# Performance work log

Hardware: AMD Instinct MI355X
Metric: run time of the kernel (lower is better)

Reference implementation:

```python
import jax, jax.numpy as jnp
import numpy as np

FIELD = 32
DIM = 64
LAYER_SIZE = (128, 128)


def setup_inputs() -> dict:
    key = jax.random.key(0)
    ks = jax.random.split(key, 5)
    B = 4096
    x = jax.random.normal(ks[0], (B, FIELD, DIM), dtype=jnp.float32)
    # conv1d kernel-size-1 weights, stored as [out_channels, in_channels]
    field_nums = [FIELD]
    params = {}
    for i, size in enumerate(LAYER_SIZE):
        in_ch = field_nums[-1] * field_nums[0]
        fan = 1.0 / np.sqrt(in_ch)
        params[f"w{i}"] = jax.random.uniform(ks[1 + 2 * i % 4], (size, in_ch), minval=-fan, maxval=fan, dtype=jnp.float32)
        params[f"b{i}"] = jax.random.uniform(ks[2 + 2 * i % 4], (size,), minval=-fan, maxval=fan, dtype=jnp.float32)
        field_nums.append(size // 2)
    return {"cin_inputs": x, "w0": params["w0"], "b0": params["b0"], "w1": params["w1"], "b1": params["b1"]}


def _cin(x, weights, biases):
    # x: [B, F, D]
    B, F, D = x.shape
    hidden = x
    finals = []
    n_layers = len(weights)
    for i, (w, b) in enumerate(zip(weights, biases)):
        size = w.shape[0]
        # outer product over field dims: [B, H, F, D] -> reshape to [B, H*F, D]
        z = jnp.einsum('bhd,bfd->bhfd', hidden, x).reshape(B, hidden.shape[1] * F, D)
        # 1x1 conv over channel dim == per-position matmul
        y = jnp.einsum('bcd,oc->bod', z, w) + b[None, :, None]
        y = jax.nn.relu(y)
        if i != n_layers - 1:
            hidden, direct = y[:, : size // 2, :], y[:, size // 2 :, :]
        else:
            direct = y
        finals.append(direct)
    return jnp.concatenate(finals, axis=1).sum(-1)  # [B, out_dim]


def reference(cin_inputs, w0, b0, w1, b1):
    return _cin(cin_inputs, [w0, w1], [b0, b1])
```

## Files before the change

### kernel.cpp

```cpp
#include <hip/hip_runtime.h>
#include <hip/hip_fp16.h>


typedef __attribute__((ext_vector_type(8))) _Float16 f16x8;
typedef __attribute__((ext_vector_type(4))) float f32x4;
typedef __attribute__((ext_vector_type(4))) unsigned short us4;
typedef unsigned short ushortT;

__device__ __forceinline__ int hidx(int o, int d) {
    return o * 64 + (d ^ ((o & 7) << 3));
}

__global__ void cin_pack_w(const float* __restrict__ w0,
                           const float* __restrict__ w1,
                           ushortT* __restrict__ wp) {
    int gidx = blockIdx.x * 256 + threadIdx.x;
    if (gidx >= 49152) return;
    const float* src;
    ushortT* dst;
    if (gidx < 16384) {
        int kk = gidx >> 9, rem = gidx & 511;
        int n = rem >> 6, lp = rem & 63;
        int o = n * 16 + (lp & 15);
        int c = kk * 32 + ((lp >> 4) << 3);
        src = w0 + o * 1024 + c;
        dst = wp + gidx * 8;
    } else {
        int g1 = gidx - 16384;
        int kk = g1 >> 9, rem = g1 & 511;
        int n = rem >> 6, lp = rem & 63;
        int o = n * 16 + (lp & 15);
        int c = kk * 32 + ((lp >> 4) << 3);
        src = w1 + o * 2048 + c;
        dst = wp + 131072 + g1 * 8;
    }
    ushortT tmp[8];
#pragma unroll
    for (int j = 0; j < 8; ++j) {
        __half h = __float2half(src[j]);
        tmp[j] = __builtin_bit_cast(ushortT, h);
    }
    *reinterpret_cast<f16x8*>(dst) = *reinterpret_cast<const f16x8*>(tmp);
}

__global__ __launch_bounds__(256, 2) void cin_mfma_kernel(
    const float* __restrict__ x,
    const float* __restrict__ b0,
    const float* __restrict__ b1,
    const ushortT* __restrict__ wp,
    float* __restrict__ out)
{
    const int tid  = threadIdx.x;
    const int l    = tid & 63;
    const int w    = tid >> 6;
    const int pair = w >> 1;
    const int nh   = w & 1;
    const int b    = blockIdx.x * 2 + pair;
    const int r16  = l & 15;
    const int g    = l >> 4;

    __shared__ ushortT U[2][4096];
    __shared__ __align__(16) ushortT Wb[2][8192];

    ushortT* Xw = U[pair];

    const float* xb = x + (size_t)b * 2048;
#pragma unroll
    for (int i = 0; i < 4; ++i) {
        const int idx = (nh * 4 + i) * 64 + l;
        float4 v = reinterpret_cast<const float4*>(xb)[idx];
        us4 h;
        h[0] = __builtin_bit_cast(ushortT, __float2half(v.x));
        h[1] = __builtin_bit_cast(ushortT, __float2half(v.y));
        h[2] = __builtin_bit_cast(ushortT, __float2half(v.z));
        h[3] = __builtin_bit_cast(ushortT, __float2half(v.w));
        *reinterpret_cast<us4*>(&Xw[idx * 4]) = h;
    }

#pragma unroll
    for (int j = 0; j < 4; ++j) {
        const int seg = w * 4 + j;
        const char* src = (const char*)wp + (size_t)seg * 1024 + (size_t)l * 16;
        __builtin_amdgcn_global_load_lds((const unsigned int*)src,
                                         (unsigned int*)&Wb[0][seg * 512], 16, 0, 0);
    }
    __syncthreads();

    __half2 tf16[4][4];
#pragma unroll
    for (int mt = 0; mt < 4; ++mt)
#pragma unroll
        for (int p = 0; p < 4; ++p) {
            unsigned lo = Xw[(g * 8 + 2 * p) * 64 + mt * 16 + r16];
            unsigned hi = Xw[(g * 8 + 2 * p + 1) * 64 + mt * 16 + r16];
            tf16[mt][p] = __builtin_bit_cast(__half2, lo | (hi << 16));
        }

    f32x4 acc[4][4];
#pragma unroll
    for (int mt = 0; mt < 4; ++mt)
#pragma unroll
        for (int n = 0; n < 4; ++n) acc[mt][n] = (f32x4){0.f, 0.f, 0.f, 0.f};

    union AfU { __half2 h2[4]; f16x8 v; };

    __half2 thc[4];
#pragma unroll
    for (int mt = 0; mt < 4; ++mt) {
        unsigned u = Xw[mt * 16 + r16];
        thc[mt] = __builtin_bit_cast(__half2, (u << 16) | u);
    }

    const int nb = nh * 4;

#pragma unroll 1
    for (int p = 0; p < 48; ++p) {
        const int ps = p & 1;
        const int k0 = 2 * p;
        const int k1 = k0 + 1;

        if (p + 1 < 48) {
#pragma unroll
            for (int j = 0; j < 4; ++j) {
                const int seg = w * 4 + j;
                const char* src = (const char*)wp + (size_t)(p + 1) * 16384 +
                                  (size_t)seg * 1024 + (size_t)l * 16;
                __builtin_amdgcn_global_load_lds((const unsigned int*)src,
                    (unsigned int*)&Wb[ps ^ 1][seg * 512], 16, 0, 0);
            }
        }

        f16x8 Bf[4];
#pragma unroll
        for (int n = 0; n < 4; ++n)
            Bf[n] = *reinterpret_cast<const f16x8*>(
                &Wb[ps][(nb + n) * 512 + l * 8]);

        AfU Af[4];
#pragma unroll
        for (int mt = 0; mt < 4; ++mt)
#pragma unroll
            for (int q = 0; q < 4; ++q)
                Af[mt].h2[q] = __hmul2(tf16[mt][q], thc[mt]);

        __half2 th1[4];
#pragma unroll
        for (int mt = 0; mt < 4; ++mt) {
            const int c = mt * 16 + r16;
            unsigned u = (k1 < 32) ? Xw[k1 * 64 + c] : Xw[hidx(k1 - 32, c)];
            th1[mt] = __builtin_bit_cast(__half2, (u << 16) | u);
        }

        __builtin_amdgcn_s_setprio(1);
#pragma unroll
        for (int n = 0; n < 4; ++n) {
#pragma unroll
            for (int mt = 0; mt < 4; ++mt)
                acc[mt][n] = __builtin_amdgcn_mfma_f32_16x16x32_f16(
                    Af[mt].v, Bf[n], acc[mt][n], 0, 0, 0);
            Bf[n] = *reinterpret_cast<const f16x8*>(
                &Wb[ps][4096 + (nb + n) * 512 + l * 8]);
        }
        __builtin_amdgcn_s_setprio(0);

#pragma unroll
        for (int mt = 0; mt < 4; ++mt)
#pragma unroll
            for (int q = 0; q < 4; ++q)
                Af[mt].h2[q] = __hmul2(tf16[mt][q], th1[mt]);

        __builtin_amdgcn_s_setprio(1);
#pragma unroll
        for (int n = 0; n < 4; ++n)
#pragma unroll
            for (int mt = 0; mt < 4; ++mt)
                acc[mt][n] = __builtin_amdgcn_mfma_f32_16x16x32_f16(
                    Af[mt].v, Bf[n], acc[mt][n], 0, 0, 0);
        __builtin_amdgcn_s_setprio(0);

        if (p + 1 < 48) {
            const int k2 = k0 + 2;
#pragma unroll
            for (int mt = 0; mt < 4; ++mt) {
                const int c = mt * 16 + r16;
                unsigned u = (k2 < 32) ? Xw[k2 * 64 + c] : Xw[hidx(k2 - 32, c)];
                thc[mt] = __builtin_bit_cast(__half2, (u << 16) | u);
            }
        }

        __syncthreads();

        if (p == 15) {
            ushortT* Hw = Xw;
            if (nh == 0) {
#pragma unroll
                for (int n = 0; n < 4; ++n) {
                    float bn = b0[n * 16 + r16];
                    const int o = n * 16 + r16;
#pragma unroll
                    for (int mt = 0; mt < 4; ++mt) {
                        us4 hv;
#pragma unroll
                        for (int r = 0; r < 4; ++r) {
                            float y = fmaxf(acc[mt][n][r] + bn, 0.f);
                            hv[r] = __builtin_bit_cast(ushortT, __float2half(y));
                        }
                        *reinterpret_cast<us4*>(&Hw[hidx(o, mt * 16 + g * 4)]) = hv;
                    }
                }
            } else {
#pragma unroll
                for (int n = 0; n < 4; ++n) {
                    float bn = b0[64 + n * 16 + r16];
                    float s = 0.f;
#pragma unroll
                    for (int mt = 0; mt < 4; ++mt)
#pragma unroll
                        for (int r = 0; r < 4; ++r)
                            s += fmaxf(acc[mt][n][r] + bn, 0.f);
                    s += __shfl_xor(s, 16);
                    s += __shfl_xor(s, 32);
                    if (l < 16) out[(size_t)b * 192 + n * 16 + l] = s;
                }
            }
#pragma unroll
            for (int mt = 0; mt < 4; ++mt)
#pragma unroll
                for (int n = 0; n < 4; ++n) acc[mt][n] = (f32x4){0.f, 0.f, 0.f, 0.f};

            __syncthreads();

#pragma unroll
            for (int mt = 0; mt < 4; ++mt) {
                unsigned u = Hw[hidx(0, mt * 16 + r16)];
                thc[mt] = __builtin_bit_cast(__half2, (u << 16) | u);
            }
        }
    }

#pragma unroll
    for (int n = 0; n < 4; ++n) {
        float bn = b1[(nb + n) * 16 + r16];
        float s = 0.f;
#pragma unroll
        for (int mt = 0; mt < 4; ++mt)
#pragma unroll
            for (int r = 0; r < 4; ++r)
                s += fmaxf(acc[mt][n][r] + bn, 0.f);
        s += __shfl_xor(s, 16);
        s += __shfl_xor(s, 32);
        if (l < 16) out[(size_t)b * 192 + 64 + (nb + n) * 16 + l] = s;
    }
}

__global__ __launch_bounds__(256, 4) void cin_fp32_kernel(
    const float* __restrict__ x, const float* __restrict__ w0,
    const float* __restrict__ b0, const float* __restrict__ w1,
    const float* __restrict__ b1, float* __restrict__ out)
{
    const int b = blockIdx.x;
    const int tid = threadIdx.x;
    const int d = tid & 63;
    const int wave = tid >> 6;

    __shared__ float Xs[32][64];
    __shared__ float Hsf[64][64];

    const float* xb = x + (size_t)b * 2048;
    float treg[32];
#pragma unroll
    for (int f = 0; f < 32; ++f) treg[f] = xb[f * 64 + d];
    if (wave == 0) {
#pragma unroll
        for (int f = 0; f < 32; ++f) Xs[f][d] = treg[f];
    }
    __syncthreads();
    const int o_base = __builtin_amdgcn_readfirstlane(wave * 32);

    for (int oi = 0; oi < 32; ++oi) {
        const int o = o_base + oi;
        const float* wrow = w0 + (size_t)o * 1024;
        float acc = b0[o];
        for (int h = 0; h < 32; ++h) {
            const float* wv = wrow + h * 32;
            const float th = Xs[h][d];
            float s0 = 0.f, s1 = 0.f, s2 = 0.f, s3 = 0.f;
#pragma unroll
            for (int f = 0; f < 32; f += 4) {
                s0 = fmaf(wv[f + 0], treg[f + 0], s0);
                s1 = fmaf(wv[f + 1], treg[f + 1], s1);
                s2 = fmaf(wv[f + 2], treg[f + 2], s2);
                s3 = fmaf(wv[f + 3], treg[f + 3], s3);
            }
            acc = fmaf((s0 + s1) + (s2 + s3), th, acc);
        }
        float y = fmaxf(acc, 0.f);
        if (o < 64) {
            Hsf[o][d] = y;
        } else {
#pragma unroll
            for (int off = 32; off > 0; off >>= 1) y += __shfl_xor(y, off, 64);
            if (d == 0) out[(size_t)b * 192 + (o - 64)] = y;
        }
    }
    __syncthreads();

    for (int oi = 0; oi < 32; ++oi) {
        const int o = o_base + oi;
        const float* wrow = w1 + (size_t)o * 2048;
        float acc = b1[o];
        for (int h = 0; h < 64; ++h) {
            const float* wv = wrow + h * 32;
            const float th = Hsf[h][d];
            float s0 = 0.f, s1 = 0.f, s2 = 0.f, s3 = 0.f;
#pragma unroll
            for (int f = 0; f < 32; f += 4) {
                s0 = fmaf(wv[f + 0], treg[f + 0], s0);
                s1 = fmaf(wv[f + 1], treg[f + 1], s1);
                s2 = fmaf(wv[f + 2], treg[f + 2], s2);
                s3 = fmaf(wv[f + 3], treg[f + 3], s3);
            }
            acc = fmaf((s0 + s1) + (s2 + s3), th, acc);
        }
        float y = fmaxf(acc, 0.f);
#pragma unroll
        for (int off = 32; off > 0; off >>= 1) y += __shfl_xor(y, off, 64);
        if (d == 0) out[(size_t)b * 192 + 64 + o] = y;
    }
}

extern "C" void kernel_launch(void* const* d_in, const int* in_sizes, int n_in,
                              void* d_out, int out_size, void* d_ws, size_t ws_size,
                              hipStream_t stream) {
    const float* x  = (const float*)d_in[0];
    const float* w0 = (const float*)d_in[1];
    const float* b0 = (const float*)d_in[2];
    const float* w1 = (const float*)d_in[3];
    const float* b1 = (const float*)d_in[4];
    float* out = (float*)d_out;

    if (ws_size >= 786432) {
        ushortT* wp = (ushortT*)d_ws;
        cin_pack_w<<<192, 256, 0, stream>>>(w0, w1, wp);
        cin_mfma_kernel<<<2048, 256, 0, stream>>>(x, b0, b1, wp, out);
    } else {
        cin_fp32_kernel<<<4096, 256, 0, stream>>>(x, w0, b0, w1, b1, out);
    }
}
```

Baseline: 190.9 us.

## Split MFMA work across waves by D-columns instead of output channels

Each wave in a pair now owns half of the D dimension (two 16-column tiles) and all eight output-channel tiles, instead of all four D tiles and half of the output channels. This halves the A-fragment construction work (hmul2 per wave) and the per-wave theta loads, but every wave now reads all eight B fragments from LDS. The direct-path sums are reduced across the two waves through a small shared scratch buffer with an extra barrier.

```diff
diff --git a/kernel.cpp b/kernel.cpp
--- a/kernel.cpp
+++ b/kernel.cpp
@@ -54,20 +54,21 @@
     const int l    = tid & 63;
     const int w    = tid >> 6;
     const int pair = w >> 1;
-    const int nh   = w & 1;
+    const int mh   = w & 1;
     const int b    = blockIdx.x * 2 + pair;
     const int r16  = l & 15;
     const int g    = l >> 4;
 
     __shared__ ushortT U[2][4096];
     __shared__ __align__(16) ushortT Wb[2][8192];
+    __shared__ float Scr[2][8][16];
 
     ushortT* Xw = U[pair];
 
     const float* xb = x + (size_t)b * 2048;
 #pragma unroll
     for (int i = 0; i < 4; ++i) {
-        const int idx = (nh * 4 + i) * 64 + l;
+        const int idx = (mh * 4 + i) * 64 + l;
         float4 v = reinterpret_cast<const float4*>(xb)[idx];
         us4 h;
         h[0] = __builtin_bit_cast(ushortT, __float2half(v.x));
@@ -86,32 +87,35 @@
     }
     __syncthreads();
 
-    __half2 tf16[4][4];
-#pragma unroll
-    for (int mt = 0; mt < 4; ++mt)
+    const int c0 = mh * 32 + r16;
+    const int c1 = mh * 32 + 16 + r16;
+
+    __half2 tf16[2][4];
+#pragma unroll
+    for (int mtl = 0; mtl < 2; ++mtl) {
+        const int c = (mtl == 0) ? c0 : c1;
 #pragma unroll
         for (int p = 0; p < 4; ++p) {
-            unsigned lo = Xw[(g * 8 + 2 * p) * 64 + mt * 16 + r16];
-            unsigned hi = Xw[(g * 8 + 2 * p + 1) * 64 + mt * 16 + r16];
-            tf16[mt][p] = __builtin_bit_cast(__half2, lo | (hi << 16));
-        }
-
-    f32x4 acc[4][4];
-#pragma unroll
-    for (int mt = 0; mt < 4; ++mt)
-#pragma unroll
-        for (int n = 0; n < 4; ++n) acc[mt][n] = (f32x4){0.f, 0.f, 0.f, 0.f};
+            unsigned lo = Xw[(g * 8 + 2 * p) * 64 + c];
+            unsigned hi = Xw[(g * 8 + 2 * p + 1) * 64 + c];
+            tf16[mtl][p] = __builtin_bit_cast(__half2, lo | (hi << 16));
+        }
+    }
+
+    f32x4 acc[2][8];
+#pragma unroll
+    for (int mtl = 0; mtl < 2; ++mtl)
+#pragma unroll
+        for (int n = 0; n < 8; ++n) acc[mtl][n] = (f32x4){0.f, 0.f, 0.f, 0.f};
 
     union AfU { __half2 h2[4]; f16x8 v; };
 
-    __half2 thc[4];
-#pragma unroll
-    for (int mt = 0; mt < 4; ++mt) {
-        unsigned u = Xw[mt * 16 + r16];
-        thc[mt] = __builtin_bit_cast(__half2, (u << 16) | u);
-    }
-
-    const int nb = nh * 4;
+    __half2 thc[2];
+    {
+        unsigned u0 = Xw[c0], u1 = Xw[c1];
+        thc[0] = __builtin_bit_cast(__half2, (u0 << 16) | u0);
+        thc[1] = __builtin_bit_cast(__half2, (u1 << 16) | u1);
+    }
 
 #pragma unroll 1
     for (int p = 0; p < 48; ++p) {
@@ -130,126 +134,135 @@
             }
         }
 
-        f16x8 Bf[4];
-#pragma unroll
-        for (int n = 0; n < 4; ++n)
+        f16x8 Bf[8];
+#pragma unroll
+        for (int n = 0; n < 8; ++n)
+            Bf[n] = *reinterpret_cast<const f16x8*>(&Wb[ps][n * 512 + l * 8]);
+
+        AfU Af[2];
+#pragma unroll
+        for (int mtl = 0; mtl < 2; ++mtl)
+#pragma unroll
+            for (int q = 0; q < 4; ++q)
+                Af[mtl].h2[q] = __hmul2(tf16[mtl][q], thc[mtl]);
+
+        __half2 th1[2];
+        {
+            unsigned u0 = (k1 < 32) ? Xw[k1 * 64 + c0] : Xw[hidx(k1 - 32, c0)];
+            unsigned u1 = (k1 < 32) ? Xw[k1 * 64 + c1] : Xw[hidx(k1 - 32, c1)];
+            th1[0] = __builtin_bit_cast(__half2, (u0 << 16) | u0);
+            th1[1] = __builtin_bit_cast(__half2, (u1 << 16) | u1);
+        }
+
+        __builtin_amdgcn_s_setprio(1);
+#pragma unroll
+        for (int n = 0; n < 8; ++n) {
+#pragma unroll
+            for (int mtl = 0; mtl < 2; ++mtl)
+                acc[mtl][n] = __builtin_amdgcn_mfma_f32_16x16x32_f16(
+                    Af[mtl].v, Bf[n], acc[mtl][n], 0, 0, 0);
             Bf[n] = *reinterpret_cast<const f16x8*>(
-                &Wb[ps][(nb + n) * 512 + l * 8]);
-
-        AfU Af[4];
-#pragma unroll
-        for (int mt = 0; mt < 4; ++mt)
+                &Wb[ps][4096 + n * 512 + l * 8]);
+        }
+        __builtin_amdgcn_s_setprio(0);
+
+#pragma unroll
+        for (int mtl = 0; mtl < 2; ++mtl)
 #pragma unroll
             for (int q = 0; q < 4; ++q)
-                Af[mt].h2[q] = __hmul2(tf16[mt][q], thc[mt]);
-
-        __half2 th1[4];
-#pragma unroll
-        for (int mt = 0; mt < 4; ++mt) {
-            const int c = mt * 16 + r16;
-            unsigned u = (k1 < 32) ? Xw[k1 * 64 + c] : Xw[hidx(k1 - 32, c)];
-            th1[mt] = __builtin_bit_cast(__half2, (u << 16) | u);
-        }
+                Af[mtl].h2[q] = __hmul2(tf16[mtl][q], th1[mtl]);
 
         __builtin_amdgcn_s_setprio(1);
 #pragma unroll
-        for (int n = 0; n < 4; ++n) {
-#pragma unroll
-            for (int mt = 0; mt < 4; ++mt)
-                acc[mt][n] = __builtin_amdgcn_mfma_f32_16x16x32_f16(
-                    Af[mt].v, Bf[n], acc[mt][n], 0, 0, 0);
-            Bf[n] = *reinterpret_cast<const f16x8*>(
-                &Wb[ps][4096 + (nb + n) * 512 + l * 8]);
-        }
-        __builtin_amdgcn_s_setprio(0);
-
-#pragma unroll
-        for (int mt = 0; mt < 4; ++mt)
-#pragma unroll
-            for (int q = 0; q < 4; ++q)
-                Af[mt].h2[q] = __hmul2(tf16[mt][q], th1[mt]);
-
-        __builtin_amdgcn_s_setprio(1);
-#pragma unroll
-        for (int n = 0; n < 4; ++n)
-#pragma unroll
-            for (int mt = 0; mt < 4; ++mt)
-                acc[mt][n] = __builtin_amdgcn_mfma_f32_16x16x32_f16(
-                    Af[mt].v, Bf[n], acc[mt][n], 0, 0, 0);
+        for (int n = 0; n < 8; ++n)
+#pragma unroll
+            for (int mtl = 0; mtl < 2; ++mtl)
+                acc[mtl][n] = __builtin_amdgcn_mfma_f32_16x16x32_f16(
+                    Af[mtl].v, Bf[n], acc[mtl][n], 0, 0, 0);
         __builtin_amdgcn_s_setprio(0);
 
         if (p + 1 < 48) {
             const int k2 = k0 + 2;
-#pragma unroll
-            for (int mt = 0; mt < 4; ++mt) {
-                const int c = mt * 16 + r16;
-                unsigned u = (k2 < 32) ? Xw[k2 * 64 + c] : Xw[hidx(k2 - 32, c)];
-                thc[mt] = __builtin_bit_cast(__half2, (u << 16) | u);
-            }
+            unsigned u0 = (k2 < 32) ? Xw[k2 * 64 + c0] : Xw[hidx(k2 - 32, c0)];
+            unsigned u1 = (k2 < 32) ? Xw[k2 * 64 + c1] : Xw[hidx(k2 - 32, c1)];
+            thc[0] = __builtin_bit_cast(__half2, (u0 << 16) | u0);
+            thc[1] = __builtin_bit_cast(__half2, (u1 << 16) | u1);
         }
 
         __syncthreads();
 
         if (p == 15) {
             ushortT* Hw = Xw;
-            if (nh == 0) {
-#pragma unroll
-                for (int n = 0; n < 4; ++n) {
-                    float bn = b0[n * 16 + r16];
-                    const int o = n * 16 + r16;
-#pragma unroll
-                    for (int mt = 0; mt < 4; ++mt) {
-                        us4 hv;
-#pragma unroll
-                        for (int r = 0; r < 4; ++r) {
-                            float y = fmaxf(acc[mt][n][r] + bn, 0.f);
-                            hv[r] = __builtin_bit_cast(ushortT, __float2half(y));
-                        }
-                        *reinterpret_cast<us4*>(&Hw[hidx(o, mt * 16 + g * 4)]) = hv;
+#pragma unroll
+            for (int n = 0; n < 4; ++n) {
+                float bn = b0[n * 16 + r16];
+                const int o = n * 16 + r16;
+#pragma unroll
+                for (int mtl = 0; mtl < 2; ++mtl) {
+                    us4 hv;
+#pragma unroll
+                    for (int r = 0; r < 4; ++r) {
+                        float y = fmaxf(acc[mtl][n][r] + bn, 0.f);
+                        hv[r] = __builtin_bit_cast(ushortT, __float2half(y));
                     }
+                    const int d0 = mh * 32 + mtl * 16 + g * 4;
+                    *reinterpret_cast<us4*>(&Hw[hidx(o, d0)]) = hv;
                 }
-            } else {
-#pragma unroll
-                for (int n = 0; n < 4; ++n) {
-                    float bn = b0[64 + n * 16 + r16];
-                    float s = 0.f;
-#pragma unroll
-                    for (int mt = 0; mt < 4; ++mt)
-#pragma unroll
-                        for (int r = 0; r < 4; ++r)
-                            s += fmaxf(acc[mt][n][r] + bn, 0.f);
-                    s += __shfl_xor(s, 16);
-                    s += __shfl_xor(s, 32);
-                    if (l < 16) out[(size_t)b * 192 + n * 16 + l] = s;
-                }
-            }
-#pragma unroll
-            for (int mt = 0; mt < 4; ++mt)
-#pragma unroll
-                for (int n = 0; n < 4; ++n) acc[mt][n] = (f32x4){0.f, 0.f, 0.f, 0.f};
-
+            }
+            float sdir[4];
+#pragma unroll
+            for (int n = 4; n < 8; ++n) {
+                float bn = b0[64 + (n - 4) * 16 + r16];
+                float s = 0.f;
+#pragma unroll
+                for (int mtl = 0; mtl < 2; ++mtl)
+#pragma unroll
+                    for (int r = 0; r < 4; ++r)
+                        s += fmaxf(acc[mtl][n][r] + bn, 0.f);
+                s += __shfl_xor(s, 16);
+                s += __shfl_xor(s, 32);
+                sdir[n - 4] = s;
+                if (mh == 1 && l < 16) Scr[pair][n][l] = s;
+            }
             __syncthreads();
-
-#pragma unroll
-            for (int mt = 0; mt < 4; ++mt) {
-                unsigned u = Hw[hidx(0, mt * 16 + r16)];
-                thc[mt] = __builtin_bit_cast(__half2, (u << 16) | u);
-            }
-        }
-    }
-
-#pragma unroll
-    for (int n = 0; n < 4; ++n) {
-        float bn = b1[(nb + n) * 16 + r16];
-        float s = 0.f;
-#pragma unroll
-        for (int mt = 0; mt < 4; ++mt)
-#pragma unroll
-            for (int r = 0; r < 4; ++r)
-                s += fmaxf(acc[mt][n][r] + bn, 0.f);
-        s += __shfl_xor(s, 16);
-        s += __shfl_xor(s, 32);
-        if (l < 16) out[(size_t)b * 192 + 64 + (nb + n) * 16 + l] = s;
+            if (mh == 0 && l < 16) {
+#pragma unroll
+                for (int n = 4; n < 8; ++n)
+                    out[(size_t)b * 192 + (n - 4) * 16 + l] =
+                        sdir[n - 4] + Scr[pair][n][l];
+            }
+#pragma unroll
+            for (int mtl = 0; mtl < 2; ++mtl)
+#pragma unroll
+                for (int n = 0; n < 8; ++n) acc[mtl][n] = (f32x4){0.f, 0.f, 0.f, 0.f};
+            unsigned u0 = Hw[hidx(0, c0)], u1 = Hw[hidx(0, c1)];
+            thc[0] = __builtin_bit_cast(__half2, (u0 << 16) | u0);
+            thc[1] = __builtin_bit_cast(__half2, (u1 << 16) | u1);
+        }
+    }
+
+    {
+        float sv[8];
+#pragma unroll
+        for (int n = 0; n < 8; ++n) {
+            float bn = b1[n * 16 + r16];
+            float s = 0.f;
+#pragma unroll
+            for (int mtl = 0; mtl < 2; ++mtl)
+#pragma unroll
+                for (int r = 0; r < 4; ++r)
+                    s += fmaxf(acc[mtl][n][r] + bn, 0.f);
+            s += __shfl_xor(s, 16);
+            s += __shfl_xor(s, 32);
+            sv[n] = s;
+            if (mh == 1 && l < 16) Scr[pair][n][l] = s;
+        }
+        __syncthreads();
+        if (mh == 0 && l < 16) {
+#pragma unroll
+            for (int n = 0; n < 8; ++n)
+                out[(size_t)b * 192 + 64 + n * 16 + l] = sv[n] + Scr[pair][n][l];
+        }
     }
 }
 
```

Measured after the change: 185.7 us. 1.03x faster.
